# Optimization experiments

Hardware: AMD Instinct MI355X
Metric: run time of the kernel (lower is better)

Reference implementation:

```python
import jax, jax.numpy as jnp
import numpy as np

N = 100000
E = 1600000
IN_DIM = 128  # m + 2 with m = 126
NEG_SLOPE_ATT = 0.2   # PyG GATConv default
NEG_SLOPE_ACT = 0.01  # F.leaky_relu default


def _gat_layer(x, src, dst, w_src, w_dst, a_src, a_dst, bias, heads, out_ch):
    n = x.shape[0]
    xs = (x @ w_src).reshape(n, heads, out_ch)  # [N,H,C]
    xd = (x @ w_dst).reshape(n, heads, out_ch)
    al_s = (xs * a_src).sum(-1)  # [N,H]
    al_d = (xd * a_dst).sum(-1)  # [N,H]
    e = jax.nn.leaky_relu(al_s[src] + al_d[dst], NEG_SLOPE_ATT)  # [E,H]
    e_max = jax.ops.segment_max(e, dst, num_segments=n)          # [N,H]
    ex = jnp.exp(e - e_max[dst])
    den = jax.ops.segment_sum(ex, dst, num_segments=n)           # [N,H]
    alpha = ex / den[dst]                                        # [E,H]
    msg = xs[src] * alpha[:, :, None]                            # [E,H,C]
    out = jax.ops.segment_sum(msg, dst, num_segments=n)          # [N,H,C]
    return out.reshape(n, heads * out_ch) + bias


def setup_inputs() -> dict:
    key = jax.random.key(0)
    ks = jax.random.split(key, 16)
    x = jax.random.normal(ks[0], (N, IN_DIM), dtype=jnp.float32)
    edge_index = jax.random.randint(ks[1], (2, E), 0, N, dtype=jnp.int64)

    def lin(k, din, dout):
        return 0.001 * jax.random.normal(k, (din, dout), dtype=jnp.float32)

    def att(k, h, c):
        return 0.1 * jax.random.normal(k, (1, h, c), dtype=jnp.float32)

    return {
        "x": x, "edge_index": edge_index,
        "w1_src": lin(ks[2], IN_DIM, 128), "w1_dst": lin(ks[3], IN_DIM, 128),
        "a1_src": att(ks[4], 8, 16), "a1_dst": att(ks[5], 8, 16),
        "b1": jnp.zeros((128,), jnp.float32),
        "w2_src": lin(ks[6], 128, 128), "w2_dst": lin(ks[7], 128, 128),
        "a2_src": att(ks[8], 8, 16), "a2_dst": att(ks[9], 8, 16),
        "b2": jnp.zeros((128,), jnp.float32),
        "w3_src": lin(ks[10], 128, 2), "w3_dst": lin(ks[11], 128, 2),
        "a3_src": att(ks[12], 1, 2), "a3_dst": att(ks[13], 1, 2),
        "b3": jnp.zeros((2,), jnp.float32),
    }


def reference(x, edge_index,
              w1_src, w1_dst, a1_src, a1_dst, b1,
              w2_src, w2_dst, a2_src, a2_dst, b2,
              w3_src, w3_dst, a3_src, a3_dst, b3):
    n = x.shape[0]
    # add_self_loops=True (PyG default)
    loops = jnp.arange(n, dtype=edge_index.dtype)
    src = jnp.concatenate([edge_index[0], loops])
    dst = jnp.concatenate([edge_index[1], loops])

    h = _gat_layer(x, src, dst, w1_src, w1_dst, a1_src, a1_dst, b1, 8, 16)
    h = jax.nn.leaky_relu(h, NEG_SLOPE_ACT)  # dropout is identity in eval
    h = _gat_layer(h, src, dst, w2_src, w2_dst, a2_src, a2_dst, b2, 8, 16)
    h = jax.nn.leaky_relu(h, NEG_SLOPE_ACT)
    out = _gat_layer(h, src, dst, w3_src, w3_dst, a3_src, a3_dst, b3, 1, 2)
    return out
```

## Files before the change

### kernel.cpp

```cpp
#include <hip/hip_runtime.h>
#include <hip/hip_bf16.h>

#define LEAKY_ATT 0.2f
#define LEAKY_ACT 0.01f
#define BSHIFT 8
#define CH 4096

typedef __attribute__((ext_vector_type(8))) short bf16x8;
typedef __attribute__((ext_vector_type(4))) float f32x4;

__device__ __forceinline__ float leaky(float x, float s) { return x >= 0.f ? x : s * x; }

__device__ __forceinline__ uint f2bf(float f) {
  __hip_bfloat16 h = __float2bfloat16(f);
  return (uint)*reinterpret_cast<ushort*>(&h);
}

__device__ __forceinline__ float bf_lo(uint q) { return __uint_as_float(q << 16); }
__device__ __forceinline__ float bf_hi(uint q) { return __uint_as_float(q & 0xffff0000u); }

__global__ __launch_bounds__(256) void k_bhist(const int* __restrict__ dst, int e, int nb,
                                               int* __restrict__ bcnt) {
  __shared__ int cnt[512];
  for (int i = threadIdx.x; i < 512; i += 256) cnt[i] = 0;
  __syncthreads();
  for (int i = blockIdx.x * 256 + threadIdx.x; i < e; i += gridDim.x * 256)
    atomicAdd(&cnt[dst[i] >> BSHIFT], 1);
  __syncthreads();
  for (int i = threadIdx.x; i < nb; i += 256)
    if (cnt[i]) atomicAdd(&bcnt[i], cnt[i]);
}

__global__ __launch_bounds__(512) void k_bscan(const int* __restrict__ bcnt, int nb,
                                               int* __restrict__ bbase, int* __restrict__ bcur) {
  __shared__ int sh[512];
  int t = threadIdx.x;
  int orig = (t < nb) ? bcnt[t] : 0;
  sh[t] = orig;
  __syncthreads();
  for (int off = 1; off < 512; off <<= 1) {
    int v = (t >= off) ? sh[t - off] : 0;
    __syncthreads();
    sh[t] += v;
    __syncthreads();
  }
  if (t < nb) {
    int ex = sh[t] - orig;
    bbase[t] = ex;
    bcur[t] = ex;
    if (t == nb - 1) bbase[nb] = sh[t];
  }
}

__global__ __launch_bounds__(256) void k_bucket(const int* __restrict__ src,
                                                const int* __restrict__ dst, int e, int nb,
                                                int* __restrict__ bcur, uint* __restrict__ bpair) {
  __shared__ uint spair[CH];
  __shared__ ushort skey[CH];
  __shared__ ushort srank[CH];
  __shared__ int cnt[512];
  __shared__ int gb[512];
  int t = threadIdx.x;
  int c0 = blockIdx.x * CH;
  int cn = min(CH, e - c0);
  if (cn <= 0) return;
  for (int i = t; i < 512; i += 256) cnt[i] = 0;
  __syncthreads();
  for (int i = t; i < cn; i += 256) {
    int s = src[c0 + i];
    int d = dst[c0 + i];
    int k = d >> BSHIFT;
    spair[i] = ((uint)(d & ((1 << BSHIFT) - 1)) << 20) | (uint)s;
    skey[i] = (ushort)k;
    srank[i] = (ushort)atomicAdd(&cnt[k], 1);
  }
  __syncthreads();
  for (int k = t; k < nb; k += 256)
    gb[k] = cnt[k] ? atomicAdd(&bcur[k], cnt[k]) : 0;
  __syncthreads();
  for (int i = t; i < cn; i += 256) {
    bpair[gb[skey[i]] + srank[i]] = spair[i];
  }
}

__global__ __launch_bounds__(256) void k_csr(const uint* __restrict__ bpair,
                                             const int* __restrict__ bbase, int n,
                                             int* __restrict__ rowptr, int* __restrict__ col) {
  __shared__ int deg[256];
  __shared__ int cur[256];
  int b = blockIdx.x, t = threadIdx.x;
  int e0 = bbase[b], e1 = bbase[b + 1];
  deg[t] = 0;
  __syncthreads();
  for (int i = e0 + t; i < e1; i += 256)
    atomicAdd(&deg[bpair[i] >> 20], 1);
  __syncthreads();
  int v = deg[t];
  cur[t] = v;
  __syncthreads();
  for (int off = 1; off < 256; off <<= 1) {
    int u = (t >= off) ? cur[t - off] : 0;
    __syncthreads();
    cur[t] += u;
    __syncthreads();
  }
  int incl = cur[t];
  int gnode = b * 256 + t;
  if (gnode < n) rowptr[gnode + 1] = e0 + incl;
  if (b == 0 && t == 0) rowptr[0] = 0;
  __syncthreads();
  cur[t] = e0 + incl - v;
  __syncthreads();
  for (int i = e0 + t; i < e1; i += 256) {
    uint pk = bpair[i];
    int loc = pk >> 20;
    int p = atomicAdd(&cur[loc], 1);
    col[p] = (int)(pk & 0xFFFFFu);
  }
}

__global__ void k_prep_vsd(const float* __restrict__ wsrc, const float* __restrict__ wdst,
                           const float* __restrict__ asrc, const float* __restrict__ adst,
                           float* __restrict__ vsd) {
  int k = blockIdx.x;
  int i = threadIdx.x;
  float s = 0.f;
  if (i < 8) {
    for (int c = 0; c < 16; ++c) s += wsrc[k * 128 + i * 16 + c] * asrc[i * 16 + c];
  } else {
    int h = i - 8;
    for (int c = 0; c < 16; ++c) s += wdst[k * 128 + h * 16 + c] * adst[h * 16 + c];
  }
  vsd[k * 16 + i] = s;
}

__global__ void k_prep_u3(const float* __restrict__ w3s, const float* __restrict__ w3d,
                          const float* __restrict__ a3s, const float* __restrict__ a3d,
                          float* __restrict__ U) {
  int k = blockIdx.x * blockDim.x + threadIdx.x;
  if (k >= 128) return;
  U[k * 4 + 0] = w3s[k * 2 + 0];
  U[k * 4 + 1] = w3s[k * 2 + 1];
  U[k * 4 + 2] = w3s[k * 2 + 0] * a3s[0] + w3s[k * 2 + 1] * a3s[1];
  U[k * 4 + 3] = w3d[k * 2 + 0] * a3d[0] + w3d[k * 2 + 1] * a3d[1];
}

__global__ __launch_bounds__(64) void k_prep_frag(const float* __restrict__ W,
                                                  const float* __restrict__ VSD,
                                                  ushort* __restrict__ WF) {
  int blk = blockIdx.x;
  int lane = threadIdx.x;
  int ct = blk >> 2, ks = blk & 3;
  uint out[4];
#pragma unroll
  for (int jj = 0; jj < 8; ++jj) {
    int k = ks * 32 + (lane >> 4) * 8 + jj;
    int c = ct * 16 + (lane & 15);
    float v = (c < 128) ? W[k * 128 + c] : VSD[k * 16 + (c - 128)];
    ((ushort*)out)[jj] = (ushort)f2bf(v);
  }
  *reinterpret_cast<uint4*>(&WF[(size_t)(blk * 64 + lane) * 8]) = *reinterpret_cast<uint4*>(out);
}

template <int INMODE>
__global__ __launch_bounds__(256) void k_gemm_mfma(const void* __restrict__ Xv,
                                                   const ushort* __restrict__ WF,
                                                   ushort* __restrict__ XSb,
                                                   float* __restrict__ AL, int n) {
  __shared__ __align__(16) char xt[16384];
  int t = threadIdx.x;
  int row0 = blockIdx.x * 64;

  if (INMODE == 0) {
    const float* X = (const float*)Xv;
#pragma unroll
    for (int i = 0; i < 8; ++i) {
      int flat = (i * 256 + t) * 4;
      int r = flat >> 7, k0 = flat & 127;
      int gr = row0 + r;
      float4 v = (gr < n) ? *reinterpret_cast<const float4*>(&X[(size_t)gr * 128 + k0])
                          : make_float4(0.f, 0.f, 0.f, 0.f);
      uint lo = f2bf(v.x) | (f2bf(v.y) << 16);
      uint hi = f2bf(v.z) | (f2bf(v.w) << 16);
      int byte = (r * 256 + k0 * 2) ^ ((r & 7) << 4);
      *reinterpret_cast<uint2*>(xt + byte) = make_uint2(lo, hi);
    }
  } else {
    const ushort* X = (const ushort*)Xv;
#pragma unroll
    for (int i = 0; i < 4; ++i) {
      int flat = (i * 256 + t) * 8;
      int r = flat >> 7, k0 = flat & 127;
      int gr = row0 + r;
      uint4 v = (gr < n) ? *reinterpret_cast<const uint4*>(&X[(size_t)gr * 128 + k0])
                         : make_uint4(0u, 0u, 0u, 0u);
      int byte = (r * 256 + k0 * 2) ^ ((r & 7) << 4);
      *reinterpret_cast<uint4*>(xt + byte) = v;
    }
  }
  __syncthreads();

  int wave = t >> 6;
  int lane = t & 63;
  int arow = wave * 16 + (lane & 15);
  int kgrp = (lane >> 4) * 8;

  bf16x8 afrag[4];
#pragma unroll
  for (int ks = 0; ks < 4; ++ks) {
    int kb = ks * 32 + kgrp;
    int byte = (arow * 256 + kb * 2) ^ ((arow & 7) << 4);
    afrag[ks] = *reinterpret_cast<const bf16x8*>(xt + byte);
  }

  f32x4 acc[9];
#pragma unroll
  for (int ct = 0; ct < 9; ++ct) {
    f32x4 a = {0.f, 0.f, 0.f, 0.f};
#pragma unroll
    for (int ks = 0; ks < 4; ++ks) {
      bf16x8 b = *reinterpret_cast<const bf16x8*>(&WF[(size_t)((ct * 4 + ks) * 64 + lane) * 8]);
      a = __builtin_amdgcn_mfma_f32_16x16x32_bf16(afrag[ks], b, a, 0, 0, 0);
    }
    acc[ct] = a;
  }

  int rbase = wave * 16 + (lane >> 4) * 4;
  int csub = lane & 15;
#pragma unroll
  for (int ct = 0; ct < 8; ++ct) {
#pragma unroll
    for (int i = 0; i < 4; ++i) {
      int gr = row0 + rbase + i;
      if (gr < n) XSb[(size_t)gr * 128 + ct * 16 + csub] = (ushort)f2bf(acc[ct][i]);
    }
  }
#pragma unroll
  for (int i = 0; i < 4; ++i) {
    int gr = row0 + rbase + i;
    if (gr < n) AL[(size_t)gr * 16 + csub] = acc[8][i];
  }
}

template <int MODE>
__global__ __launch_bounds__(256) void k_gat_agg(const ushort* __restrict__ XSb,
                                                 const float* __restrict__ AL,
                                                 const int* __restrict__ rowptr,
                                                 const int* __restrict__ col,
                                                 const float* __restrict__ bias,
                                                 void* __restrict__ OUTv,
                                                 const float* __restrict__ U, int n) {
  int t = threadIdx.x;
  int lane = t & 63;
  int node = blockIdx.x * 4 + (t >> 6);
  if (node >= n) return;
  int sub = lane & 31;
  int g = lane >> 5;
  int hd = sub >> 2;
  int c0 = sub * 4;

  float ald = AL[(size_t)node * 16 + 8 + hd];

  float w0 = __expf(leaky(AL[(size_t)node * 16 + hd] + ald, LEAKY_ATT));
  if (g != 0) w0 = 0.f;
  uint2 qs = *reinterpret_cast<const uint2*>(&XSb[(size_t)node * 128 + c0]);
  float acc0 = w0 * bf_lo(qs.x);
  float acc1 = w0 * bf_hi(qs.x);
  float acc2 = w0 * bf_lo(qs.y);
  float acc3 = w0 * bf_hi(qs.y);
  float den = w0;

  int beg = rowptr[node], end = rowptr[node + 1];
  int base = beg;
  for (; base + 4 <= end; base += 4) {
    int s0 = col[base + g];
    int s1 = col[base + 2 + g];
    float l0 = AL[(size_t)s0 * 16 + hd];
    float l1 = AL[(size_t)s1 * 16 + hd];
    uint2 q0 = *reinterpret_cast<const uint2*>(&XSb[(size_t)s0 * 128 + c0]);
    uint2 q1 = *reinterpret_cast<const uint2*>(&XSb[(size_t)s1 * 128 + c0]);
    float wa = __expf(leaky(l0 + ald, LEAKY_ATT));
    float wb = __expf(leaky(l1 + ald, LEAKY_ATT));
    acc0 += wa * bf_lo(q0.x);
    acc1 += wa * bf_hi(q0.x);
    acc2 += wa * bf_lo(q0.y);
    acc3 += wa * bf_hi(q0.y);
    den += wa;
    acc0 += wb * bf_lo(q1.x);
    acc1 += wb * bf_hi(q1.x);
    acc2 += wb * bf_lo(q1.y);
    acc3 += wb * bf_hi(q1.y);
    den += wb;
  }
  for (; base < end; base += 2) {
    int idx = base + g;
    bool on = idx < end;
    int s = on ? col[idx] : node;
    float l = AL[(size_t)s * 16 + hd];
    uint2 q = *reinterpret_cast<const uint2*>(&XSb[(size_t)s * 128 + c0]);
    float w = on ? __expf(leaky(l + ald, LEAKY_ATT)) : 0.f;
    acc0 += w * bf_lo(q.x);
    acc1 += w * bf_hi(q.x);
    acc2 += w * bf_lo(q.y);
    acc3 += w * bf_hi(q.y);
    den += w;
  }

  acc0 += __shfl_xor(acc0, 32);
  acc1 += __shfl_xor(acc1, 32);
  acc2 += __shfl_xor(acc2, 32);
  acc3 += __shfl_xor(acc3, 32);
  den += __shfl_xor(den, 32);

  if (g == 0) {
    float inv = 1.f / den;
    float4 bv = *reinterpret_cast<const float4*>(&bias[c0]);
    float r0 = leaky(acc0 * inv + bv.x, LEAKY_ACT);
    float r1 = leaky(acc1 * inv + bv.y, LEAKY_ACT);
    float r2 = leaky(acc2 * inv + bv.z, LEAKY_ACT);
    float r3 = leaky(acc3 * inv + bv.w, LEAKY_ACT);
    if (MODE == 1) {
      ushort* HB = (ushort*)OUTv;
      uint lo = f2bf(r0) | (f2bf(r1) << 16);
      uint hi = f2bf(r2) | (f2bf(r3) << 16);
      *reinterpret_cast<uint2*>(&HB[(size_t)node * 128 + c0]) = make_uint2(lo, hi);
    } else {
      float rr[4] = {r0, r1, r2, r3};
      float p0 = 0.f, p1 = 0.f, p2 = 0.f, p3 = 0.f;
#pragma unroll
      for (int c = 0; c < 4; ++c) {
        float4 uv = *reinterpret_cast<const float4*>(&U[(c0 + c) * 4]);
        p0 += rr[c] * uv.x;
        p1 += rr[c] * uv.y;
        p2 += rr[c] * uv.z;
        p3 += rr[c] * uv.w;
      }
#pragma unroll
      for (int m = 1; m < 32; m <<= 1) {
        p0 += __shfl_xor(p0, m);
        p1 += __shfl_xor(p1, m);
        p2 += __shfl_xor(p2, m);
        p3 += __shfl_xor(p3, m);
      }
      if (sub == 0) {
        float* X3 = (float*)OUTv;
        *reinterpret_cast<float4*>(&X3[(size_t)node * 4]) = make_float4(p0, p1, p2, p3);
      }
    }
  }
}

__global__ __launch_bounds__(256) void k_agg3(const float* __restrict__ XSAL3,
                                              const int* __restrict__ rowptr,
                                              const int* __restrict__ col,
                                              const float* __restrict__ b3,
                                              float* __restrict__ out, int n) {
  int node = blockIdx.x * blockDim.x + threadIdx.x;
  if (node >= n) return;
  float4 self = *reinterpret_cast<const float4*>(&XSAL3[node * 4]);
  float ald = self.w;
  float e0 = leaky(self.z + ald, LEAKY_ATT);
  float w0 = __expf(e0);
  float den = w0;
  float a0 = w0 * self.x;
  float a1 = w0 * self.y;
  int end = rowptr[node + 1];
  for (int jj = rowptr[node]; jj < end; ++jj) {
    int s = col[jj];
    float4 v = *reinterpret_cast<const float4*>(&XSAL3[s * 4]);
    float ee = leaky(v.z + ald, LEAKY_ATT);
    float w = __expf(ee);
    den += w;
    a0 += w * v.x;
    a1 += w * v.y;
  }
  out[node * 2 + 0] = a0 / den + b3[0];
  out[node * 2 + 1] = a1 / den + b3[1];
}

extern "C" void kernel_launch(void* const* d_in, const int* in_sizes, int n_in,
                              void* d_out, int out_size, void* d_ws, size_t ws_size,
                              hipStream_t stream) {
  const float* x = (const float*)d_in[0];
  const int* ei = (const int*)d_in[1];
  const float* w1s = (const float*)d_in[2];
  const float* w1d = (const float*)d_in[3];
  const float* a1s = (const float*)d_in[4];
  const float* a1d = (const float*)d_in[5];
  const float* b1 = (const float*)d_in[6];
  const float* w2s = (const float*)d_in[7];
  const float* w2d = (const float*)d_in[8];
  const float* a2s = (const float*)d_in[9];
  const float* a2d = (const float*)d_in[10];
  const float* b2 = (const float*)d_in[11];
  const float* w3s = (const float*)d_in[12];
  const float* w3d = (const float*)d_in[13];
  const float* a3s = (const float*)d_in[14];
  const float* a3d = (const float*)d_in[15];
  const float* b3 = (const float*)d_in[16];

  int n = in_sizes[0] / 128;
  int e = in_sizes[1] / 2;
  const int* srcp = ei;
  const int* dstp = ei + e;

  int nb = (n + 255) >> BSHIFT;
  if (nb > 512) return;
  if (n >= (1 << 20)) return;

  size_t off = 0;
  auto alloc = [&](size_t bytes) -> void* {
    void* p = (char*)d_ws + off;
    off += (bytes + 255) & ~(size_t)255;
    return p;
  };
  int* bcnt = (int*)alloc((size_t)nb * 4);
  int* bbase = (int*)alloc((size_t)(nb + 1) * 4);
  int* bcur = (int*)alloc((size_t)nb * 4);
  uint* bpair = (uint*)alloc((size_t)e * 4);
  int* rowptr = (int*)alloc((size_t)(n + 1) * 4);
  int* col = (int*)alloc((size_t)e * 4);
  float* vsd1 = (float*)alloc(128 * 16 * 4);
  float* vsd2 = (float*)alloc(128 * 16 * 4);
  float* u3 = (float*)alloc(128 * 4 * 4);
  ushort* wf1 = (ushort*)alloc(36 * 64 * 8 * 2);
  ushort* wf2 = (ushort*)alloc(36 * 64 * 8 * 2);
  float* al = (float*)alloc((size_t)n * 16 * 4);
  ushort* xsb = (ushort*)alloc((size_t)n * 128 * 2);
  ushort* hb = (ushort*)alloc((size_t)n * 128 * 2);
  float* xsal3 = (float*)alloc((size_t)n * 4 * 4);
  if (off > ws_size) return;

  hipMemsetAsync(bcnt, 0, (size_t)nb * 4, stream);
  k_bhist<<<512, 256, 0, stream>>>(dstp, e, nb, bcnt);
  k_bscan<<<1, 512, 0, stream>>>(bcnt, nb, bbase, bcur);
  k_bucket<<<(e + CH - 1) / CH, 256, 0, stream>>>(srcp, dstp, e, nb, bcur, bpair);
  k_csr<<<nb, 256, 0, stream>>>(bpair, bbase, n, rowptr, col);

  k_prep_vsd<<<128, 16, 0, stream>>>(w1s, w1d, a1s, a1d, vsd1);
  k_prep_vsd<<<128, 16, 0, stream>>>(w2s, w2d, a2s, a2d, vsd2);
  k_prep_u3<<<1, 128, 0, stream>>>(w3s, w3d, a3s, a3d, u3);
  k_prep_frag<<<36, 64, 0, stream>>>(w1s, vsd1, wf1);
  k_prep_frag<<<36, 64, 0, stream>>>(w2s, vsd2, wf2);

  int gb = (n + 63) / 64;
  int ab = (n + 3) / 4;
  k_gemm_mfma<0><<<gb, 256, 0, stream>>>(x, wf1, xsb, al, n);
  k_gat_agg<1><<<ab, 256, 0, stream>>>(xsb, al, rowptr, col, b1, hb, nullptr, n);
  k_gemm_mfma<1><<<gb, 256, 0, stream>>>(hb, wf2, xsb, al, n);
  k_gat_agg<2><<<ab, 256, 0, stream>>>(xsb, al, rowptr, col, b2, xsal3, u3, n);
  k_agg3<<<(n + 255) / 256, 256, 0, stream>>>(xsal3, rowptr, col, b3, (float*)d_out, n);
}
```

Before: 309.7 us.

## Split GAT aggregation into per-edge weight pass and head-sliced gather kernels

Projected features are stored head-major (one 16-channel slab per head), and attention logits are split into separate source and destination arrays. A new pass precomputes per-edge, per-head exp weights as fp16, and the aggregation runs one block group per head so each gather touches a compact 32-byte slab that is more likely to stay in cache. The layer-3 projection moves out of the layer-2 aggregation into its own kernel, and agg3 is unrolled by four. The cost is an extra kernel per layer, reading and writing an 8×E fp16 weight array, an eightfold larger aggregation grid that reloads col and rowptr once per head, and some loss of precision in the fp16 weights.

```diff
diff --git a/kernel.cpp b/kernel.cpp
--- a/kernel.cpp
+++ b/kernel.cpp
@@ -1,5 +1,6 @@
 #include <hip/hip_runtime.h>
 #include <hip/hip_bf16.h>
+#include <hip/hip_fp16.h>
 
 #define LEAKY_ATT 0.2f
 #define LEAKY_ACT 0.01f
@@ -9,7 +10,7 @@
 typedef __attribute__((ext_vector_type(8))) short bf16x8;
 typedef __attribute__((ext_vector_type(4))) float f32x4;
 
-__device__ __forceinline__ float leaky(float x, float s) { return x >= 0.f ? x : s * x; }
+__device__ __forceinline__ float lrelu(float x, float s) { return fmaxf(x, s * x); }
 
 __device__ __forceinline__ uint f2bf(float f) {
   __hip_bfloat16 h = __float2bfloat16(f);
@@ -18,6 +19,15 @@
 
 __device__ __forceinline__ float bf_lo(uint q) { return __uint_as_float(q << 16); }
 __device__ __forceinline__ float bf_hi(uint q) { return __uint_as_float(q & 0xffff0000u); }
+
+__device__ __forceinline__ ushort f2h(float f) {
+  __half h = __float2half(f);
+  return *reinterpret_cast<ushort*>(&h);
+}
+__device__ __forceinline__ float h2f(ushort u) {
+  __half h = *reinterpret_cast<__half*>(&u);
+  return __half2float(h);
+}
 
 __global__ __launch_bounds__(256) void k_bhist(const int* __restrict__ dst, int e, int nb,
                                                int* __restrict__ bcnt) {
@@ -165,8 +175,9 @@
 template <int INMODE>
 __global__ __launch_bounds__(256) void k_gemm_mfma(const void* __restrict__ Xv,
                                                    const ushort* __restrict__ WF,
-                                                   ushort* __restrict__ XSb,
-                                                   float* __restrict__ AL, int n) {
+                                                   ushort* __restrict__ XSH,
+                                                   float* __restrict__ ALS,
+                                                   float* __restrict__ ALD, int n) {
   __shared__ __align__(16) char xt[16384];
   int t = threadIdx.x;
   int row0 = blockIdx.x * 64;
@@ -232,122 +243,159 @@
 #pragma unroll
     for (int i = 0; i < 4; ++i) {
       int gr = row0 + rbase + i;
-      if (gr < n) XSb[(size_t)gr * 128 + ct * 16 + csub] = (ushort)f2bf(acc[ct][i]);
+      if (gr < n)
+        XSH[(size_t)ct * n * 16 + (size_t)gr * 16 + csub] = (ushort)f2bf(acc[ct][i]);
     }
   }
 #pragma unroll
   for (int i = 0; i < 4; ++i) {
     int gr = row0 + rbase + i;
-    if (gr < n) AL[(size_t)gr * 16 + csub] = acc[8][i];
-  }
-}
-
-template <int MODE>
-__global__ __launch_bounds__(256) void k_gat_agg(const ushort* __restrict__ XSb,
-                                                 const float* __restrict__ AL,
-                                                 const int* __restrict__ rowptr,
-                                                 const int* __restrict__ col,
-                                                 const float* __restrict__ bias,
-                                                 void* __restrict__ OUTv,
-                                                 const float* __restrict__ U, int n) {
+    if (gr < n) {
+      float v = acc[8][i];
+      if (csub < 8) ALS[(size_t)gr * 8 + csub] = v;
+      else ALD[(size_t)gr * 8 + (csub - 8)] = v;
+    }
+  }
+}
+
+__global__ __launch_bounds__(256) void k_passw(const float* __restrict__ ALS,
+                                               const float* __restrict__ ALD,
+                                               const int* __restrict__ rowptr,
+                                               const int* __restrict__ col,
+                                               ushort* __restrict__ w8h, int n, int E) {
   int t = threadIdx.x;
   int lane = t & 63;
   int node = blockIdx.x * 4 + (t >> 6);
   if (node >= n) return;
-  int sub = lane & 31;
-  int g = lane >> 5;
-  int hd = sub >> 2;
+  int e4 = lane >> 2, cq = lane & 3;
+  float2 ad = *reinterpret_cast<const float2*>(ALD + (size_t)node * 8 + cq * 2);
+  int beg = __builtin_nontemporal_load(rowptr + node);
+  int end = __builtin_nontemporal_load(rowptr + node + 1);
+  for (int base = beg; base < end; base += 32) {
+    int i0 = base + e4, i1 = base + 16 + e4;
+    bool on0 = i0 < end, on1 = i1 < end;
+    int ci0 = on0 ? i0 : beg, ci1 = on1 ? i1 : beg;
+    int s0 = __builtin_nontemporal_load(col + ci0);
+    int s1 = __builtin_nontemporal_load(col + ci1);
+    float2 as0 = *reinterpret_cast<const float2*>(ALS + (size_t)s0 * 8 + cq * 2);
+    float2 as1 = *reinterpret_cast<const float2*>(ALS + (size_t)s1 * 8 + cq * 2);
+    if (on0) {
+      ushort u0 = f2h(__expf(lrelu(as0.x + ad.x, LEAKY_ATT)));
+      ushort u1 = f2h(__expf(lrelu(as0.y + ad.y, LEAKY_ATT)));
+      __builtin_nontemporal_store(u0, w8h + (size_t)(cq * 2) * E + i0);
+      __builtin_nontemporal_store(u1, w8h + (size_t)(cq * 2 + 1) * E + i0);
+    }
+    if (on1) {
+      ushort u0 = f2h(__expf(lrelu(as1.x + ad.x, LEAKY_ATT)));
+      ushort u1 = f2h(__expf(lrelu(as1.y + ad.y, LEAKY_ATT)));
+      __builtin_nontemporal_store(u0, w8h + (size_t)(cq * 2) * E + i1);
+      __builtin_nontemporal_store(u1, w8h + (size_t)(cq * 2 + 1) * E + i1);
+    }
+  }
+}
+
+__global__ __launch_bounds__(256) void k_aggs(const ushort* __restrict__ XSH,
+                                              const ushort* __restrict__ w8h,
+                                              const float* __restrict__ ALS,
+                                              const float* __restrict__ ALD,
+                                              const int* __restrict__ rowptr,
+                                              const int* __restrict__ col,
+                                              const float* __restrict__ bias,
+                                              ushort* __restrict__ HB, int n, int E) {
+  int t = threadIdx.x;
+  int lane = t & 63;
+  int bid = blockIdx.x;
+  int h = bid & 7;
+  int node = (bid >> 3) * 4 + (t >> 6);
+  if (node >= n) return;
+  int e4 = lane >> 2, cq = lane & 3;
+  const char* XHb = (const char*)XSH + (size_t)h * n * 32;
+  const ushort* wz = w8h + (size_t)h * E;
+
+  float w0 = __expf(lrelu(ALS[(size_t)node * 8 + h] + ALD[(size_t)node * 8 + h], LEAKY_ATT));
+  float sw = (e4 == 0) ? w0 : 0.f;
+  uint2 qs = *(const uint2*)(XHb + ((uint)node * 32 + cq * 8));
+  float a0 = sw * bf_lo(qs.x), a1 = sw * bf_hi(qs.x);
+  float a2 = sw * bf_lo(qs.y), a3 = sw * bf_hi(qs.y);
+  float den = sw;
+
+  int beg = __builtin_nontemporal_load(rowptr + node);
+  int end = __builtin_nontemporal_load(rowptr + node + 1);
+  for (int base = beg; base < end; base += 32) {
+    int i0 = base + e4, i1 = base + 16 + e4;
+    bool on0 = i0 < end, on1 = i1 < end;
+    int ci0 = on0 ? i0 : beg, ci1 = on1 ? i1 : beg;
+    int s0 = __builtin_nontemporal_load(col + ci0);
+    int s1 = __builtin_nontemporal_load(col + ci1);
+    ushort uw0 = __builtin_nontemporal_load(wz + ci0);
+    ushort uw1 = __builtin_nontemporal_load(wz + ci1);
+    uint2 q0 = *(const uint2*)(XHb + ((uint)s0 * 32 + cq * 8));
+    uint2 q1 = *(const uint2*)(XHb + ((uint)s1 * 32 + cq * 8));
+    float wA = on0 ? h2f(uw0) : 0.f;
+    float wB = on1 ? h2f(uw1) : 0.f;
+    a0 += wA * bf_lo(q0.x);
+    a1 += wA * bf_hi(q0.x);
+    a2 += wA * bf_lo(q0.y);
+    a3 += wA * bf_hi(q0.y);
+    a0 += wB * bf_lo(q1.x);
+    a1 += wB * bf_hi(q1.x);
+    a2 += wB * bf_lo(q1.y);
+    a3 += wB * bf_hi(q1.y);
+    den += wA + wB;
+  }
+
+#pragma unroll
+  for (int m = 4; m <= 32; m <<= 1) {
+    a0 += __shfl_xor(a0, m);
+    a1 += __shfl_xor(a1, m);
+    a2 += __shfl_xor(a2, m);
+    a3 += __shfl_xor(a3, m);
+    den += __shfl_xor(den, m);
+  }
+
+  if (lane < 4) {
+    int ch0 = h * 16 + lane * 4;
+    float inv = 1.f / den;
+    float4 bv = *reinterpret_cast<const float4*>(&bias[ch0]);
+    float r0 = lrelu(a0 * inv + bv.x, LEAKY_ACT);
+    float r1 = lrelu(a1 * inv + bv.y, LEAKY_ACT);
+    float r2 = lrelu(a2 * inv + bv.z, LEAKY_ACT);
+    float r3 = lrelu(a3 * inv + bv.w, LEAKY_ACT);
+    unsigned long long o =
+        (unsigned long long)(f2bf(r0) | (f2bf(r1) << 16)) |
+        ((unsigned long long)(f2bf(r2) | (f2bf(r3) << 16)) << 32);
+    __builtin_nontemporal_store(
+        o, reinterpret_cast<unsigned long long*>(&HB[(size_t)node * 128 + ch0]));
+  }
+}
+
+__global__ __launch_bounds__(256) void k_lin3b(const ushort* __restrict__ HB,
+                                               const float* __restrict__ U,
+                                               float* __restrict__ X3, int n) {
+  int t = threadIdx.x;
+  int node = blockIdx.x * 8 + (t >> 5);
+  if (node >= n) return;
+  int sub = t & 31;
+  uint2 q = *reinterpret_cast<const uint2*>(&HB[(size_t)node * 128 + sub * 4]);
+  float r0 = bf_lo(q.x), r1 = bf_hi(q.x), r2 = bf_lo(q.y), r3 = bf_hi(q.y);
   int c0 = sub * 4;
-
-  float ald = AL[(size_t)node * 16 + 8 + hd];
-
-  float w0 = __expf(leaky(AL[(size_t)node * 16 + hd] + ald, LEAKY_ATT));
-  if (g != 0) w0 = 0.f;
-  uint2 qs = *reinterpret_cast<const uint2*>(&XSb[(size_t)node * 128 + c0]);
-  float acc0 = w0 * bf_lo(qs.x);
-  float acc1 = w0 * bf_hi(qs.x);
-  float acc2 = w0 * bf_lo(qs.y);
-  float acc3 = w0 * bf_hi(qs.y);
-  float den = w0;
-
-  int beg = rowptr[node], end = rowptr[node + 1];
-  int base = beg;
-  for (; base + 4 <= end; base += 4) {
-    int s0 = col[base + g];
-    int s1 = col[base + 2 + g];
-    float l0 = AL[(size_t)s0 * 16 + hd];
-    float l1 = AL[(size_t)s1 * 16 + hd];
-    uint2 q0 = *reinterpret_cast<const uint2*>(&XSb[(size_t)s0 * 128 + c0]);
-    uint2 q1 = *reinterpret_cast<const uint2*>(&XSb[(size_t)s1 * 128 + c0]);
-    float wa = __expf(leaky(l0 + ald, LEAKY_ATT));
-    float wb = __expf(leaky(l1 + ald, LEAKY_ATT));
-    acc0 += wa * bf_lo(q0.x);
-    acc1 += wa * bf_hi(q0.x);
-    acc2 += wa * bf_lo(q0.y);
-    acc3 += wa * bf_hi(q0.y);
-    den += wa;
-    acc0 += wb * bf_lo(q1.x);
-    acc1 += wb * bf_hi(q1.x);
-    acc2 += wb * bf_lo(q1.y);
-    acc3 += wb * bf_hi(q1.y);
-    den += wb;
-  }
-  for (; base < end; base += 2) {
-    int idx = base + g;
-    bool on = idx < end;
-    int s = on ? col[idx] : node;
-    float l = AL[(size_t)s * 16 + hd];
-    uint2 q = *reinterpret_cast<const uint2*>(&XSb[(size_t)s * 128 + c0]);
-    float w = on ? __expf(leaky(l + ald, LEAKY_ATT)) : 0.f;
-    acc0 += w * bf_lo(q.x);
-    acc1 += w * bf_hi(q.x);
-    acc2 += w * bf_lo(q.y);
-    acc3 += w * bf_hi(q.y);
-    den += w;
-  }
-
-  acc0 += __shfl_xor(acc0, 32);
-  acc1 += __shfl_xor(acc1, 32);
-  acc2 += __shfl_xor(acc2, 32);
-  acc3 += __shfl_xor(acc3, 32);
-  den += __shfl_xor(den, 32);
-
-  if (g == 0) {
-    float inv = 1.f / den;
-    float4 bv = *reinterpret_cast<const float4*>(&bias[c0]);
-    float r0 = leaky(acc0 * inv + bv.x, LEAKY_ACT);
-    float r1 = leaky(acc1 * inv + bv.y, LEAKY_ACT);
-    float r2 = leaky(acc2 * inv + bv.z, LEAKY_ACT);
-    float r3 = leaky(acc3 * inv + bv.w, LEAKY_ACT);
-    if (MODE == 1) {
-      ushort* HB = (ushort*)OUTv;
-      uint lo = f2bf(r0) | (f2bf(r1) << 16);
-      uint hi = f2bf(r2) | (f2bf(r3) << 16);
-      *reinterpret_cast<uint2*>(&HB[(size_t)node * 128 + c0]) = make_uint2(lo, hi);
-    } else {
-      float rr[4] = {r0, r1, r2, r3};
-      float p0 = 0.f, p1 = 0.f, p2 = 0.f, p3 = 0.f;
-#pragma unroll
-      for (int c = 0; c < 4; ++c) {
-        float4 uv = *reinterpret_cast<const float4*>(&U[(c0 + c) * 4]);
-        p0 += rr[c] * uv.x;
-        p1 += rr[c] * uv.y;
-        p2 += rr[c] * uv.z;
-        p3 += rr[c] * uv.w;
-      }
-#pragma unroll
-      for (int m = 1; m < 32; m <<= 1) {
-        p0 += __shfl_xor(p0, m);
-        p1 += __shfl_xor(p1, m);
-        p2 += __shfl_xor(p2, m);
-        p3 += __shfl_xor(p3, m);
-      }
-      if (sub == 0) {
-        float* X3 = (float*)OUTv;
-        *reinterpret_cast<float4*>(&X3[(size_t)node * 4]) = make_float4(p0, p1, p2, p3);
-      }
-    }
-  }
+  float4 u0 = *reinterpret_cast<const float4*>(&U[(c0 + 0) * 4]);
+  float4 u1 = *reinterpret_cast<const float4*>(&U[(c0 + 1) * 4]);
+  float4 u2 = *reinterpret_cast<const float4*>(&U[(c0 + 2) * 4]);
+  float4 u3 = *reinterpret_cast<const float4*>(&U[(c0 + 3) * 4]);
+  float p0 = r0 * u0.x + r1 * u1.x + r2 * u2.x + r3 * u3.x;
+  float p1 = r0 * u0.y + r1 * u1.y + r2 * u2.y + r3 * u3.y;
+  float p2 = r0 * u0.z + r1 * u1.z + r2 * u2.z + r3 * u3.z;
+  float p3 = r0 * u0.w + r1 * u1.w + r2 * u2.w + r3 * u3.w;
+#pragma unroll
+  for (int m = 1; m <= 16; m <<= 1) {
+    p0 += __shfl_xor(p0, m);
+    p1 += __shfl_xor(p1, m);
+    p2 += __shfl_xor(p2, m);
+    p3 += __shfl_xor(p3, m);
+  }
+  if (sub == 0)
+    *reinterpret_cast<float4*>(&X3[(size_t)node * 4]) = make_float4(p0, p1, p2, p3);
 }
 
 __global__ __launch_bounds__(256) void k_agg3(const float* __restrict__ XSAL3,
@@ -357,19 +405,35 @@
                                               float* __restrict__ out, int n) {
   int node = blockIdx.x * blockDim.x + threadIdx.x;
   if (node >= n) return;
-  float4 self = *reinterpret_cast<const float4*>(&XSAL3[node * 4]);
+  const char* XB = (const char*)XSAL3;
+  float4 self = *(const float4*)(XB + ((size_t)((uint)node << 4)));
   float ald = self.w;
-  float e0 = leaky(self.z + ald, LEAKY_ATT);
-  float w0 = __expf(e0);
+  float w0 = __expf(lrelu(self.z + ald, LEAKY_ATT));
   float den = w0;
   float a0 = w0 * self.x;
   float a1 = w0 * self.y;
-  int end = rowptr[node + 1];
-  for (int jj = rowptr[node]; jj < end; ++jj) {
-    int s = col[jj];
-    float4 v = *reinterpret_cast<const float4*>(&XSAL3[s * 4]);
-    float ee = leaky(v.z + ald, LEAKY_ATT);
-    float w = __expf(ee);
+  int jj = rowptr[node], end = rowptr[node + 1];
+  for (; jj + 4 <= end; jj += 4) {
+    int sA = __builtin_nontemporal_load(col + jj);
+    int sB = __builtin_nontemporal_load(col + jj + 1);
+    int sC = __builtin_nontemporal_load(col + jj + 2);
+    int sD = __builtin_nontemporal_load(col + jj + 3);
+    float4 vA = *(const float4*)(XB + ((uint)sA << 4));
+    float4 vB = *(const float4*)(XB + ((uint)sB << 4));
+    float4 vC = *(const float4*)(XB + ((uint)sC << 4));
+    float4 vD = *(const float4*)(XB + ((uint)sD << 4));
+    float wA = __expf(lrelu(vA.z + ald, LEAKY_ATT));
+    float wB = __expf(lrelu(vB.z + ald, LEAKY_ATT));
+    float wC = __expf(lrelu(vC.z + ald, LEAKY_ATT));
+    float wD = __expf(lrelu(vD.z + ald, LEAKY_ATT));
+    a0 += wA * vA.x + wB * vB.x + wC * vC.x + wD * vD.x;
+    a1 += wA * vA.y + wB * vB.y + wC * vC.y + wD * vD.y;
+    den += (wA + wB) + (wC + wD);
+  }
+  for (; jj < end; ++jj) {
+    int s = __builtin_nontemporal_load(col + jj);
+    float4 v = *(const float4*)(XB + ((uint)s << 4));
+    float w = __expf(lrelu(v.z + ald, LEAKY_ATT));
     den += w;
     a0 += w * v.x;
     a1 += w * v.y;
@@ -417,7 +481,10 @@
   int* bcnt = (int*)alloc((size_t)nb * 4);
   int* bbase = (int*)alloc((size_t)(nb + 1) * 4);
   int* bcur = (int*)alloc((size_t)nb * 4);
-  uint* bpair = (uint*)alloc((size_t)e * 4);
+  size_t w8h_bytes = (size_t)8 * e * 2;
+  size_t bpair_bytes = (size_t)e * 4;
+  ushort* w8h = (ushort*)alloc(w8h_bytes > bpair_bytes ? w8h_bytes : bpair_bytes);
+  uint* bpair = (uint*)w8h;
   int* rowptr = (int*)alloc((size_t)(n + 1) * 4);
   int* col = (int*)alloc((size_t)e * 4);
   float* vsd1 = (float*)alloc(128 * 16 * 4);
@@ -425,13 +492,14 @@
   float* u3 = (float*)alloc(128 * 4 * 4);
   ushort* wf1 = (ushort*)alloc(36 * 64 * 8 * 2);
   ushort* wf2 = (ushort*)alloc(36 * 64 * 8 * 2);
-  float* al = (float*)alloc((size_t)n * 16 * 4);
-  ushort* xsb = (ushort*)alloc((size_t)n * 128 * 2);
+  float* als8 = (float*)alloc((size_t)n * 8 * 4);
+  float* ald8 = (float*)alloc((size_t)n * 8 * 4);
+  ushort* xsh = (ushort*)alloc((size_t)n * 128 * 2);
   ushort* hb = (ushort*)alloc((size_t)n * 128 * 2);
   float* xsal3 = (float*)alloc((size_t)n * 4 * 4);
   if (off > ws_size) return;
 
-  hipMemsetAsync(bcnt, 0, (size_t)nb * 4, stream);
+  (void)hipMemsetAsync(bcnt, 0, (size_t)nb * 4, stream);
   k_bhist<<<512, 256, 0, stream>>>(dstp, e, nb, bcnt);
   k_bscan<<<1, 512, 0, stream>>>(bcnt, nb, bbase, bcur);
   k_bucket<<<(e + CH - 1) / CH, 256, 0, stream>>>(srcp, dstp, e, nb, bcur, bpair);
@@ -444,10 +512,15 @@
   k_prep_frag<<<36, 64, 0, stream>>>(w2s, vsd2, wf2);
 
   int gb = (n + 63) / 64;
-  int ab = (n + 3) / 4;
-  k_gemm_mfma<0><<<gb, 256, 0, stream>>>(x, wf1, xsb, al, n);
-  k_gat_agg<1><<<ab, 256, 0, stream>>>(xsb, al, rowptr, col, b1, hb, nullptr, n);
-  k_gemm_mfma<1><<<gb, 256, 0, stream>>>(hb, wf2, xsb, al, n);
-  k_gat_agg<2><<<ab, 256, 0, stream>>>(xsb, al, rowptr, col, b2, xsal3, u3, n);
+  int pb = (n + 3) / 4;
+  int ab = ((n + 3) / 4) * 8;
+
+  k_gemm_mfma<0><<<gb, 256, 0, stream>>>(x, wf1, xsh, als8, ald8, n);
+  k_passw<<<pb, 256, 0, stream>>>(als8, ald8, rowptr, col, w8h, n, e);
+  k_aggs<<<ab, 256, 0, stream>>>(xsh, w8h, als8, ald8, rowptr, col, b1, hb, n, e);
+  k_gemm_mfma<1><<<gb, 256, 0, stream>>>(hb, wf2, xsh, als8, ald8, n);
+  k_passw<<<pb, 256, 0, stream>>>(als8, ald8, rowptr, col, w8h, n, e);
+  k_aggs<<<ab, 256, 0, stream>>>(xsh, w8h, als8, ald8, rowptr, col, b2, hb, n, e);
+  k_lin3b<<<(n + 7) / 8, 256, 0, stream>>>(hb, u3, xsal3, n);
   k_agg3<<<(n + 255) / 256, 256, 0, stream>>>(xsal3, rowptr, col, b3, (float*)d_out, n);
 }
```

New measurement: 805.3 us. 160% more time.
